# Performance work log

Measured on AMD Instinct MI355X. Metric: run time of the kernel, lower is better.

Reference implementation:

```python
import jax, jax.numpy as jnp
import numpy as np

SEQ, BATCH = 1024, 2
N_HEAD, D_MODEL = 16, 1024
Q_LORA, KV_LORA = 20, 20
ROPE = D_MODEL // N_HEAD // 2   # 32 qk_rope_head_dim
NOPE = D_MODEL // N_HEAD // 2   # 32 qk_nope_head_dim
V_DIM = D_MODEL // N_HEAD       # 64
N_EXP, HID = 4, 1024            # hidden_dim = d_inner//5 = 5120//5
N_GROUP, TOPK_GROUP, TOP_K = 2, 2, 1
ROUTED_SCALE = 1.0


def setup_inputs() -> dict:
    key = jax.random.key(0)
    ks = jax.random.split(key, 16)
    sc = 0.02
    return {
        'dec_inp': jax.random.normal(ks[0], (SEQ, BATCH, D_MODEL), jnp.float32),
        'wq_a': jax.random.normal(ks[1], (D_MODEL, Q_LORA), jnp.float32) * sc,
        'q_norm_w': jnp.ones((Q_LORA,), jnp.float32),
        'wq_b': jax.random.normal(ks[2], (Q_LORA, N_HEAD * (NOPE + ROPE)), jnp.float32) * sc,
        'wkv_a': jax.random.normal(ks[3], (D_MODEL, KV_LORA + ROPE), jnp.float32) * sc,
        'kv_norm_w': jnp.ones((KV_LORA,), jnp.float32),
        'wkv_b': jax.random.normal(ks[4], (KV_LORA, N_HEAD * (NOPE + V_DIM)), jnp.float32) * sc,
        'wo': jax.random.normal(ks[5], (N_HEAD * V_DIM, D_MODEL), jnp.float32) * sc,
        'gate_w': jax.random.normal(ks[6], (N_EXP, D_MODEL), jnp.float32) * sc,
        'exp_gate': jax.random.normal(ks[7], (N_EXP, D_MODEL, HID), jnp.float32) * sc,
        'exp_up': jax.random.normal(ks[8], (N_EXP, D_MODEL, HID), jnp.float32) * sc,
        'exp_down': jax.random.normal(ks[9], (N_EXP, HID, D_MODEL), jnp.float32) * sc,
        'sh_gate': jax.random.normal(ks[10], (D_MODEL, HID), jnp.float32) * sc,
        'sh_up': jax.random.normal(ks[11], (D_MODEL, HID), jnp.float32) * sc,
        'sh_down': jax.random.normal(ks[12], (HID, D_MODEL), jnp.float32) * sc,
    }


def _rms(x, w, eps=1e-6):
    return x * jax.lax.rsqrt(jnp.mean(x * x, axis=-1, keepdims=True) + eps) * w


def _freqs(seqlen):
    # precompute_freqs_cis(rope_dim * n_head, seqlen): dim = 512 here
    dim = ROPE * N_HEAD
    inv = 1.0 / (10000.0 ** (jnp.arange(0, dim, 2, dtype=jnp.float32) / dim))  # [dim//2]
    ang = jnp.arange(seqlen, dtype=jnp.float32)[:, None] * inv[None, :]       # [s, dim//2]
    ang = ang.reshape(seqlen, N_HEAD, ROPE // 2)
    return jnp.cos(ang), jnp.sin(ang)


def _rope(x, cos, sin):
    # x: [b, s, h, ROPE]; interleaved-pair complex rotation
    b, s, h, _ = x.shape
    xr = x.reshape(b, s, h, ROPE // 2, 2)
    x0, x1 = xr[..., 0], xr[..., 1]
    c = cos[None]  # [1, s, h, ROPE//2]
    sn = sin[None]
    o0 = x0 * c - x1 * sn
    o1 = x0 * sn + x1 * c
    return jnp.stack([o0, o1], axis=-1).reshape(b, s, h, ROPE)


def reference(dec_inp, wq_a, q_norm_w, wq_b, wkv_a, kv_norm_w, wkv_b, wo,
              gate_w, exp_gate, exp_up, exp_down, sh_gate, sh_up, sh_down):
    x = jnp.swapaxes(dec_inp, 0, 1)  # [b, s, d]
    b, s, d = x.shape
    # ---- MLA attention ----
    q = _rms(x @ wq_a, q_norm_w) @ wq_b                       # [b, s, h*(nope+rope)]
    q = q.reshape(b, s, N_HEAD, NOPE + ROPE)
    q_nope, q_pe = q[..., :NOPE], q[..., NOPE:]
    kv = x @ wkv_a                                            # [b, s, kv_lora+rope]
    ckv, k_pe = kv[..., :KV_LORA], kv[..., KV_LORA:]
    kvb = (_rms(ckv, kv_norm_w) @ wkv_b).reshape(b, s, N_HEAD, NOPE + V_DIM)
    k_nope, v = kvb[..., :NOPE], kvb[..., NOPE:]
    cos, sin = _freqs(s)
    q_pe = _rope(q_pe, cos, sin)
    k_pe_h = _rope(jnp.broadcast_to(k_pe[:, :, None, :], (b, s, N_HEAD, ROPE)), cos, sin)
    qf = jnp.concatenate([q_nope, q_pe], axis=-1)             # [b, s, h, 64]
    kf = jnp.concatenate([k_nope, k_pe_h], axis=-1)
    scale = 1.0 / np.sqrt(NOPE + ROPE)
    scores = jnp.einsum('bshd,bthd->bhst', qf, kf) * scale    # mask=None in the source forward
    probs = jax.nn.softmax(scores, axis=-1)
    attn = jnp.einsum('bhst,bthd->bshd', probs, v).reshape(b, s, N_HEAD * V_DIM)
    y = attn @ wo                                             # [b, s, d]
    y = jnp.swapaxes(y, 0, 1)                                 # [s, b, d]
    # ---- DeepSeekMoE (group_limited_greedy, top_k=1, 1 shared expert) ----
    xf = y.reshape(-1, d)                                     # [T, d]
    T = xf.shape[0]
    sc = jax.nn.softmax(xf @ gate_w.T, axis=-1)               # [T, E]
    gsc = sc.reshape(T, N_GROUP, N_EXP // N_GROUP).max(axis=-1)  # [T, n_group]
    _, gidx = jax.lax.top_k(gsc, TOPK_GROUP)
    gmask = jax.nn.one_hot(gidx, N_GROUP, dtype=sc.dtype).sum(axis=1)  # [T, n_group]
    smask = jnp.repeat(gmask, N_EXP // N_GROUP, axis=-1)      # [T, E]
    tw, ti = jax.lax.top_k(jnp.where(smask > 0, sc, 0.0), TOP_K)
    comb = (jax.nn.one_hot(ti, N_EXP, dtype=sc.dtype) * tw[..., None]).sum(axis=1) * ROUTED_SCALE  # [T, E]
    g = jnp.einsum('td,edh->teh', xf, exp_gate)
    u = jnp.einsum('td,edh->teh', xf, exp_up)
    dn = jnp.einsum('teh,ehd->ted', jax.nn.silu(g) * u, exp_down)
    routed = jnp.einsum('ted,te->td', dn, comb)
    shared = (jax.nn.silu(xf @ sh_gate) * (xf @ sh_up)) @ sh_down
    return (routed + shared).reshape(s, b, d)
```

## Files before the change

### kernel.cpp

```cpp
#include <hip/hip_runtime.h>
#include <hip/hip_bf16.h>
#include <math.h>

#define SEQ 1024
#define BATCH 2
#define T 2048
#define DM 1024
#define NH 16
#define NOPE 32
#define HD 64
#define QL 20
#define KVL 20
#define KVA 52
#define HID 1024
#define NEXP 4
#define LSTR 80

typedef short bf16x8 __attribute__((ext_vector_type(8)));
typedef float f32x4 __attribute__((ext_vector_type(4)));
typedef float f32x16 __attribute__((ext_vector_type(16)));
typedef __hip_bfloat16 bf16;

static __device__ __forceinline__ float sigmoidf_(float x) {
    return 1.0f / (1.0f + __expf(-x));
}
static __device__ __forceinline__ unsigned short bfbits(float x) {
    bf16 h = __float2bfloat16(x);
    return *reinterpret_cast<unsigned short*>(&h);
}
static __device__ __forceinline__ unsigned cvt_pk_bf16(float lo, float hi) {
    unsigned r;
    asm("v_cvt_pk_bf16_f32 %0, %1, %2" : "=v"(r) : "v"(lo), "v"(hi));
    return r;
}
static __device__ __forceinline__ void gload16(const bf16* g, char* l) {
    __builtin_amdgcn_global_load_lds(
        (const __attribute__((address_space(1))) unsigned int*)g,
        (__attribute__((address_space(3))) unsigned int*)l, 16, 0, 0);
}
static __device__ __forceinline__ void barrier_() {
    asm volatile("" ::: "memory");
    __builtin_amdgcn_s_barrier();
    asm volatile("" ::: "memory");
}
#define VMWAIT(N) asm volatile("s_waitcnt vmcnt(" #N ")" ::: "memory")

__global__ __launch_bounds__(256) void k_setup(
    const float* __restrict__ wo, const float* __restrict__ sg,
    const float* __restrict__ su, const float* __restrict__ sd,
    const float* __restrict__ eg, const float* __restrict__ eu,
    const float* __restrict__ ed,
    bf16* __restrict__ woT, bf16* __restrict__ sgT, bf16* __restrict__ suT,
    bf16* __restrict__ sdT, bf16* __restrict__ egT, bf16* __restrict__ euT,
    bf16* __restrict__ edT,
    const float* __restrict__ wq_a, const float* __restrict__ wkv_a,
    const float* __restrict__ wq_b, const float* __restrict__ wkv_b,
    bf16* __restrict__ loraT, bf16* __restrict__ wqbT, bf16* __restrict__ wkvbT,
    float* __restrict__ ctab, float* __restrict__ stab)
{
    int z = blockIdx.z;
    int tid = threadIdx.x;
    if (z < 16) {
        __shared__ float tile[32][33];
        const float* in; bf16* out;
        if      (z == 0) { in = wo; out = woT; }
        else if (z == 1) { in = sg; out = sgT; }
        else if (z == 2) { in = su; out = suT; }
        else if (z == 3) { in = sd; out = sdT; }
        else if (z < 8)  { size_t o = (size_t)(z - 4)  * DM * HID; in = eg + o; out = egT + o; }
        else if (z < 12) { size_t o = (size_t)(z - 8)  * DM * HID; in = eu + o; out = euT + o; }
        else             { size_t o = (size_t)(z - 12) * HID * DM; in = ed + o; out = edT + o; }
        int c0 = blockIdx.x * 32, r0 = blockIdx.y * 32;
        int tx = tid & 31, ty = tid >> 5;
        #pragma unroll
        for (int ii = 0; ii < 4; ++ii)
            tile[ty + ii * 8][tx] = in[(size_t)(r0 + ty + ii * 8) * 1024 + c0 + tx];
        __syncthreads();
        int c = tid >> 3, rg = (tid & 7) * 4;
        ushort4 o4;
        o4.x = bfbits(tile[rg + 0][c]);
        o4.y = bfbits(tile[rg + 1][c]);
        o4.z = bfbits(tile[rg + 2][c]);
        o4.w = bfbits(tile[rg + 3][c]);
        *(ushort4*)&out[(size_t)(c0 + c) * 1024 + r0 + rg] = o4;
    } else if (z == 16) {
        int s = blockIdx.y * 32 + blockIdx.x;
        int p = tid;
        float freq = exp2f(-(float)p * (13.287712379549449f / 256.0f));
        float ang = (float)s * freq;
        float sn, cs;
        __sincosf(ang, &sn, &cs);
        ctab[s * 256 + p] = cs;
        stab[s * 256 + p] = sn;
    } else {
        int idx = (blockIdx.y * 32 + blockIdx.x) * 256 + tid;
        if (z == 17) {
            if (idx >= 80 * 1024) return;
            int n = idx >> 10, k = idx & 1023;
            float v = (n < 20) ? wq_a[k * QL + n] : (n < 72 ? wkv_a[k * KVA + (n - 20)] : 0.f);
            loraT[idx] = __float2bfloat16(v);
        } else if (z == 18) {
            if (idx >= 1024 * 32) return;
            int n = idx >> 5, k = idx & 31;
            wqbT[idx] = __float2bfloat16(k < 20 ? wq_b[k * DM + n] : 0.f);
        } else {
            if (idx >= 1536 * 32) return;
            int n = idx >> 5, k = idx & 31;
            wkvbT[idx] = __float2bfloat16(k < 20 ? wkv_b[k * (NH * 96) + n] : 0.f);
        }
    }
}

__global__ __launch_bounds__(256) void k_p1(
    const float* __restrict__ dec, const bf16* __restrict__ loraT,
    float* __restrict__ lora4)
{
    __shared__ __align__(16) char As[128 * LSTR];
    __shared__ __align__(16) char Bs[80 * LSTR];
    const int tid = threadIdx.x;
    const int kz = blockIdx.x;
    const int m0 = blockIdx.y * 128;
    const int lane = tid & 63, wave = tid >> 6;
    const int g = lane >> 4, c = lane & 15;
    f32x4 acc[2][5] = {};
    for (int ks = 0; ks < 16; ++ks) {
        int k0 = kz * 512 + ks * 32;
        __syncthreads();
        #pragma unroll
        for (int pass = 0; pass < 4; ++pass) {
            int row = (tid >> 3) + pass * 32;
            int t = m0 + row;
            int b = t >> 10, s = t & 1023;
            f32x4 v = *(const f32x4*)&dec[(size_t)(s * 2 + b) * DM + k0 + (tid & 7) * 4];
            ushort4 h4;
            h4.x = bfbits(v[0]); h4.y = bfbits(v[1]);
            h4.z = bfbits(v[2]); h4.w = bfbits(v[3]);
            *(ushort4*)&As[row * LSTR + (tid & 7) * 8] = h4;
        }
        if (tid < 160) {
            int row = tid >> 1, hf = tid & 1;
            const bf16* src = &loraT[row * 1024 + k0 + hf * 16];
            *(int4*)&Bs[row * LSTR + hf * 32]      = *(const int4*)&src[0];
            *(int4*)&Bs[row * LSTR + hf * 32 + 16] = *(const int4*)&src[8];
        }
        __syncthreads();
        bf16x8 af[2], bff[5];
        #pragma unroll
        for (int mi = 0; mi < 2; ++mi)
            af[mi] = *(const bf16x8*)&As[(wave * 32 + mi * 16 + c) * LSTR + 16 * g];
        #pragma unroll
        for (int nf = 0; nf < 5; ++nf)
            bff[nf] = *(const bf16x8*)&Bs[(nf * 16 + c) * LSTR + 16 * g];
        #pragma unroll
        for (int mi = 0; mi < 2; ++mi)
            #pragma unroll
            for (int nf = 0; nf < 5; ++nf)
                acc[mi][nf] = __builtin_amdgcn_mfma_f32_16x16x32_bf16(af[mi], bff[nf], acc[mi][nf], 0, 0, 0);
    }
    #pragma unroll
    for (int mi = 0; mi < 2; ++mi)
        #pragma unroll
        for (int nf = 0; nf < 5; ++nf)
            #pragma unroll
            for (int r = 0; r < 4; ++r) {
                int col = nf * 16 + c;
                if (col < 72) {
                    int row = m0 + wave * 32 + mi * 16 + 4 * g + r;
                    lora4[((size_t)kz * T + row) * 72 + col] = acc[mi][nf][r];
                }
            }
}

__global__ __launch_bounds__(256) void k_p2m(
    const float* __restrict__ lora4, const float* __restrict__ qnw,
    const float* __restrict__ kvnw, const float* __restrict__ ctab,
    const float* __restrict__ stab, bf16* __restrict__ nrmq,
    bf16* __restrict__ nrmkv, bf16* __restrict__ kb, int* __restrict__ cnt)
{
    int bid = blockIdx.x, tid = threadIdx.x;
    if (bid == 0 && tid < 16) cnt[tid] = 0;
    {
        int t = bid, p = tid;
        int r = p & 15, h = p >> 4, s = t & (SEQ - 1);
        float y0 = lora4[t * 72 + 40 + 2 * r] + lora4[(size_t)(T + t) * 72 + 40 + 2 * r];
        float y1 = lora4[t * 72 + 41 + 2 * r] + lora4[(size_t)(T + t) * 72 + 41 + 2 * r];
        float cs = ctab[s * 256 + p], sn = stab[s * 256 + p];
        ushort2 pk;
        pk.x = bfbits(y0 * cs - y1 * sn);
        pk.y = bfbits(y0 * sn + y1 * cs);
        *(ushort2*)&kb[(size_t)t * DM + h * HD + NOPE + 2 * r] = pk;
    }
    if (bid < 8) {
        int t = bid * 256 + tid;
        float lq[20], lk[20];
        float ssq = 0.f, ssk = 0.f;
        #pragma unroll
        for (int i = 0; i < 20; ++i) {
            lq[i] = lora4[t * 72 + i] + lora4[(size_t)(T + t) * 72 + i];
            ssq += lq[i] * lq[i];
        }
        #pragma unroll
        for (int i = 0; i < 20; ++i) {
            lk[i] = lora4[t * 72 + 20 + i] + lora4[(size_t)(T + t) * 72 + 20 + i];
            ssk += lk[i] * lk[i];
        }
        float fq = rsqrtf(ssq / 20.f + 1e-6f);
        float fk = rsqrtf(ssk / 20.f + 1e-6f);
        #pragma unroll
        for (int i = 0; i < 32; ++i) {
            nrmq[t * 32 + i]  = __float2bfloat16(i < 20 ? lq[i] * fq * qnw[i]  : 0.f);
            nrmkv[t * 32 + i] = __float2bfloat16(i < 20 ? lk[i] * fk * kvnw[i] : 0.f);
        }
    }
}

__global__ __launch_bounds__(256) void k_p3(
    const bf16* __restrict__ nrmq, const bf16* __restrict__ wqbT,
    const bf16* __restrict__ nrmkv, const bf16* __restrict__ wkvbT,
    const float* __restrict__ ctab, const float* __restrict__ stab,
    bf16* __restrict__ qb, bf16* __restrict__ kb, bf16* __restrict__ vt_g)
{
    const int zq = (blockIdx.z == 0);
    if (zq && blockIdx.x >= 16) return;
    __shared__ __align__(16) char As[128 * LSTR];
    __shared__ __align__(16) char Bs[64 * LSTR];
    const int tid = threadIdx.x;
    const int m0 = blockIdx.y * 128, n0 = blockIdx.x * 64;
    const int lane = tid & 63, wave = tid >> 6;
    const int g = lane >> 4, c = lane & 15;
    const int wm = wave >> 1, wn = wave & 1;
    const bf16* nrm = zq ? nrmq : nrmkv;
    const bf16* wT  = zq ? wqbT : wkvbT;
    {
        int row = tid >> 1, hf = tid & 1;
        const bf16* sa = &nrm[(size_t)(m0 + row) * 32 + hf * 16];
        *(int4*)&As[row * LSTR + hf * 32]      = *(const int4*)&sa[0];
        *(int4*)&As[row * LSTR + hf * 32 + 16] = *(const int4*)&sa[8];
        int brow = tid >> 2;
        *(int4*)&Bs[brow * LSTR + (tid & 3) * 16] = *(const int4*)&wT[(size_t)(n0 + brow) * 32 + (tid & 3) * 8];
    }
    __syncthreads();
    f32x4 acc[4][2] = {};
    bf16x8 af[4], bfr[2];
    #pragma unroll
    for (int mi = 0; mi < 4; ++mi)
        af[mi] = *(const bf16x8*)&As[(wm * 64 + mi * 16 + c) * LSTR + 16 * g];
    #pragma unroll
    for (int ni = 0; ni < 2; ++ni)
        bfr[ni] = *(const bf16x8*)&Bs[(wn * 32 + ni * 16 + c) * LSTR + 16 * g];
    #pragma unroll
    for (int mi = 0; mi < 4; ++mi)
        #pragma unroll
        for (int ni = 0; ni < 2; ++ni)
            acc[mi][ni] = __builtin_amdgcn_mfma_f32_16x16x32_bf16(af[mi], bfr[ni], acc[mi][ni], 0, 0, 0);

    if (zq) {
        #pragma unroll
        for (int mi = 0; mi < 4; ++mi)
            #pragma unroll
            for (int ni = 0; ni < 2; ++ni) {
                #pragma unroll
                for (int r = 0; r < 4; ++r) acc[mi][ni][r] *= 0.18033688f;
                int n = n0 + wn * 32 + ni * 16 + c;
                int w = n & 63;
                if (w < 32) {
                    #pragma unroll
                    for (int r = 0; r < 4; ++r) {
                        int row = m0 + wm * 64 + mi * 16 + 4 * g + r;
                        qb[(size_t)row * DM + n] = __float2bfloat16(acc[mi][ni][r]);
                    }
                } else {
                    int h = n >> 6;
                    int pidx = h * 16 + ((w - 32) >> 1);
                    int odd = w & 1;
                    #pragma unroll
                    for (int r = 0; r < 4; ++r) {
                        int row = m0 + wm * 64 + mi * 16 + 4 * g + r;
                        int s = row & (SEQ - 1);
                        float own = acc[mi][ni][r];
                        float oth = __shfl_xor(own, 1);
                        float cs = ctab[s * 256 + pidx], sn = stab[s * 256 + pidx];
                        float o = odd ? (oth * sn + own * cs) : (own * cs - oth * sn);
                        qb[(size_t)row * DM + n] = __float2bfloat16(o);
                    }
                }
            }
    } else {
        #pragma unroll
        for (int mi = 0; mi < 4; ++mi)
            #pragma unroll
            for (int ni = 0; ni < 2; ++ni) {
                int n = n0 + wn * 32 + ni * 16 + c;
                int h = n / 96, w = n - h * 96;
                int row0 = m0 + wm * 64 + mi * 16 + 4 * g;
                if (w < NOPE) {
                    #pragma unroll
                    for (int r = 0; r < 4; ++r)
                        kb[(size_t)(row0 + r) * DM + h * HD + w] = __float2bfloat16(acc[mi][ni][r]);
                } else {
                    int d = w - NOPE;
                    int b = row0 >> 10, s0 = row0 & (SEQ - 1);
                    ushort4 v4;
                    v4.x = bfbits(acc[mi][ni][0]);
                    v4.y = bfbits(acc[mi][ni][1]);
                    v4.z = bfbits(acc[mi][ni][2]);
                    v4.w = bfbits(acc[mi][ni][3]);
                    *(ushort4*)&vt_g[(((size_t)(b * NH + h) * HD + d) << 10) + s0] = v4;
                }
            }
    }
}

__global__ __launch_bounds__(512) void k_attn(
    const bf16* __restrict__ qb, const bf16* __restrict__ kb,
    const bf16* __restrict__ vt_g, bf16* __restrict__ ab)
{
    __shared__ __align__(16) char stage[2][16384];
    __shared__ float pol[4][32][65];
    __shared__ float mll[4][32][2];

    const int qt = blockIdx.x, h = blockIdx.y, b = blockIdx.z;
    const int tid = threadIdx.x;
    const int lane = tid & 63, wave = tid >> 6;
    const int l31 = lane & 31, hi = lane >> 5;
    const int sp = wave >> 2, wq = wave & 3;
    const int q0 = qt * 128 + wq * 32;
    char* ks = stage[sp];
    char* vt = stage[sp] + 8192;
    const int ptid = tid & 255;

    bf16x8 qf[4];
    {
        const bf16* qrow = &qb[(size_t)(b * SEQ + q0 + l31) * DM + h * HD + 8 * hi];
        #pragma unroll
        for (int st = 0; st < 4; ++st)
            qf[st] = *(const bf16x8*)&qrow[16 * st];
    }

    f32x16 o0 = {}, o1 = {};
    float m_run = -3.0e38f, l_run = 0.f;
    const size_t vbase = ((size_t)(b * NH + h) * HD) << 10;

    for (int ktl = 0; ktl < 8; ++ktl) {
        const int kt = sp * 8 + ktl;
        __syncthreads();
        #pragma unroll
        for (int ps = 0; ps < 2; ++ps) {
            int row = (ptid >> 3) + ps * 32;
            int col8 = (ptid & 7) * 8;
            int sw = (col8 * 2) ^ ((row & 7) << 4);
            int4 kv4 = *(const int4*)&kb[(size_t)(b * SEQ + kt * 64 + row) * DM + h * HD + col8];
            *(int4*)&ks[row * 128 + sw] = kv4;
            int4 vv4 = *(const int4*)&vt_g[vbase + ((size_t)row << 10) + kt * 64 + col8];
            *(int4*)&vt[row * 128 + sw] = vv4;
        }
        __syncthreads();

        f32x16 sc0 = {}, sc1 = {};
        #pragma unroll
        for (int st = 0; st < 4; ++st) {
            int colb = 32 * st + 16 * hi;
            int r0 = l31;
            bf16x8 kf0 = *(const bf16x8*)&ks[r0 * 128 + (colb ^ ((r0 & 7) << 4))];
            sc0 = __builtin_amdgcn_mfma_f32_32x32x16_bf16(kf0, qf[st], sc0, 0, 0, 0);
            int r1 = 32 + l31;
            bf16x8 kf1 = *(const bf16x8*)&ks[r1 * 128 + (colb ^ ((r1 & 7) << 4))];
            sc1 = __builtin_amdgcn_mfma_f32_32x32x16_bf16(kf1, qf[st], sc1, 0, 0, 0);
        }

        float mt = fmaxf(sc0[0], sc1[0]);
        #pragma unroll
        for (int i = 1; i < 16; ++i) mt = fmaxf(mt, fmaxf(sc0[i], sc1[i]));
        mt = fmaxf(mt, __shfl_xor(mt, 32));

        if (!__all(mt <= m_run + 8.0f)) {
            float m_new = fmaxf(m_run, mt);
            float corr = exp2f(m_run - m_new);
            m_run = m_new;
            l_run *= corr;
            #pragma unroll
            for (int i = 0; i < 16; ++i) { o0[i] *= corr; o1[i] *= corr; }
        }
        float ls = 0.f;
        #pragma unroll
        for (int i = 0; i < 16; ++i) {
            sc0[i] = exp2f(sc0[i] - m_run);
            sc1[i] = exp2f(sc1[i] - m_run);
            ls += sc0[i] + sc1[i];
        }
        ls += __shfl_xor(ls, 32);
        l_run += ls;

        unsigned pk0[8], pk1[8];
        #pragma unroll
        for (int i = 0; i < 8; ++i) {
            pk0[i] = cvt_pk_bf16(sc0[2 * i], sc0[2 * i + 1]);
            pk1[i] = cvt_pk_bf16(sc1[2 * i], sc1[2 * i + 1]);
        }

#define PV_SUB(PK, KK)                                                          \
        {                                                                       \
            _Pragma("unroll")                                                   \
            for (int s = 0; s < 2; ++s) {                                       \
                unsigned sx = hi ? PK[4*s]   : PK[4*s+2];                       \
                unsigned rx = __shfl_xor(sx, 32);                               \
                unsigned sy = hi ? PK[4*s+1] : PK[4*s+3];                       \
                unsigned ry = __shfl_xor(sy, 32);                               \
                int4 bi;                                                        \
                bi.x = hi ? (int)rx : (int)PK[4*s];                             \
                bi.y = hi ? (int)ry : (int)PK[4*s+1];                           \
                bi.z = hi ? (int)PK[4*s+2] : (int)rx;                           \
                bi.w = hi ? (int)PK[4*s+3] : (int)ry;                           \
                bf16x8 bfr = *(bf16x8*)&bi;                                     \
                int cb = (KK) * 64 + 32 * s + 16 * hi;                          \
                {                                                               \
                    int vr = l31;                                               \
                    bf16x8 vf = *(const bf16x8*)&vt[vr * 128 + (cb ^ ((vr & 7) << 4))]; \
                    o0 = __builtin_amdgcn_mfma_f32_32x32x16_bf16(vf, bfr, o0, 0, 0, 0); \
                }                                                               \
                {                                                               \
                    int vr = 32 + l31;                                          \
                    bf16x8 vf = *(const bf16x8*)&vt[vr * 128 + (cb ^ ((vr & 7) << 4))]; \
                    o1 = __builtin_amdgcn_mfma_f32_32x32x16_bf16(vf, bfr, o1, 0, 0, 0); \
                }                                                               \
            }                                                                   \
        }
        PV_SUB(pk0, 0)
        PV_SUB(pk1, 1)
#undef PV_SUB
    }

    if (sp == 1) {
        #pragma unroll
        for (int i = 0; i < 16; ++i) {
            int d = (i & 3) + 8 * (i >> 2) + 4 * hi;
            pol[wq][l31][d]      = o0[i];
            pol[wq][l31][32 + d] = o1[i];
        }
        if (hi == 0) { mll[wq][l31][0] = m_run; mll[wq][l31][1] = l_run; }
    }
    __syncthreads();
    if (sp == 1) return;

    float m_b = mll[wq][l31][0], l_b = mll[wq][l31][1];
    float M = fmaxf(m_run, m_b);
    float wa = exp2f(m_run - M), wb = exp2f(m_b - M);
    float inv = 1.0f / (l_run * wa + l_b * wb);
    #pragma unroll
    for (int i = 0; i < 16; ++i) {
        int d = (i & 3) + 8 * (i >> 2) + 4 * hi;
        o0[i] = (o0[i] * wa + pol[wq][l31][d]      * wb) * inv;
        o1[i] = (o1[i] * wa + pol[wq][l31][32 + d] * wb) * inv;
    }

    char* tb = stage[0] + wq * 8192;
    #pragma unroll
    for (int i = 0; i < 8; ++i) {
        int dbase = 2 * (i & 1) + 8 * (i >> 1) + 4 * hi;
        *(unsigned*)&tb[l31 * 140 + (dbase) * 2]      = cvt_pk_bf16(o0[2 * i], o0[2 * i + 1]);
        *(unsigned*)&tb[l31 * 140 + (32 + dbase) * 2] = cvt_pk_bf16(o1[2 * i], o1[2 * i + 1]);
    }
    __builtin_amdgcn_s_waitcnt(0);
    #pragma unroll
    for (int p = 0; p < 8; ++p) {
        int idx = p * 64 + lane;
        int q = idx >> 4, c8 = idx & 15;
        int2 rv;
        rv.x = *(const int*)&tb[q * 140 + c8 * 8];
        rv.y = *(const int*)&tb[q * 140 + c8 * 8 + 4];
        *(int2*)&ab[(size_t)(b * SEQ + q0 + q) * DM + h * HD + c8 * 4] = rv;
    }
}

__global__ __launch_bounds__(512) void k_mm_plain(
    const bf16* __restrict__ A, const bf16* __restrict__ Bt, bf16* __restrict__ C)
{
    __shared__ __align__(16) char As[2][8192];
    __shared__ __align__(16) char Bs[2][4096];
    const int tid = threadIdx.x;
    const int lane = tid & 63, wave = tid >> 6;
    const int g = lane >> 4, c = lane & 15;
    const int wm = wave >> 1, wn = wave & 1;
    const int m0 = blockIdx.y * 128, n0 = blockIdx.x * 64;

    const int ldr = lane >> 2;
    const int ldc = (lane & 3) * 8;
    const bf16* agp = &A[(size_t)(m0 + wave * 16 + ldr) * DM + ldc];
    const bool doB = wave >= 4;
    const bf16* bgp = &Bt[(size_t)(n0 + (wave & 3) * 16 + ldr) * DM + ldc];
    const int aoffL = wave * 1024, boffL = (wave & 3) * 1024;

    f32x4 acc[2][2] = {};
    const int NT = DM / 32;
    gload16(agp, As[0] + aoffL);
    if (doB) gload16(bgp, Bs[0] + boffL);
    for (int k = 0; k < NT; ++k) {
        const int cur = k & 1;
        if (k + 1 < NT) {
            gload16(agp + (k + 1) * 32, As[cur ^ 1] + aoffL);
            if (doB) gload16(bgp + (k + 1) * 32, Bs[cur ^ 1] + boffL);
            if (doB) VMWAIT(2); else VMWAIT(1);
        } else {
            VMWAIT(0);
        }
        barrier_();
        bf16x8 af[2], bfx[2];
        #pragma unroll
        for (int mi = 0; mi < 2; ++mi)
            af[mi] = *(const bf16x8*)&As[cur][(wm * 32 + mi * 16 + c) * 64 + g * 16];
        #pragma unroll
        for (int ni = 0; ni < 2; ++ni)
            bfx[ni] = *(const bf16x8*)&Bs[cur][(wn * 32 + ni * 16 + c) * 64 + g * 16];
        #pragma unroll
        for (int mi = 0; mi < 2; ++mi)
            #pragma unroll
            for (int ni = 0; ni < 2; ++ni)
                acc[mi][ni] = __builtin_amdgcn_mfma_f32_16x16x32_bf16(af[mi], bfx[ni], acc[mi][ni], 0, 0, 0);
        barrier_();
    }
    #pragma unroll
    for (int mi = 0; mi < 2; ++mi)
        #pragma unroll
        for (int ni = 0; ni < 2; ++ni)
            #pragma unroll
            for (int r = 0; r < 4; ++r)
                C[(size_t)(m0 + wm * 32 + mi * 16 + 4 * g + r) * DM + n0 + wn * 32 + ni * 16 + c]
                    = __float2bfloat16(acc[mi][ni][r]);
}

__global__ __launch_bounds__(512) void k_mm_gu_all(
    const bf16* __restrict__ X, const bf16* __restrict__ egT,
    const bf16* __restrict__ euT, const bf16* __restrict__ sgT,
    const bf16* __restrict__ suT, const int* __restrict__ cnt,
    const int* __restrict__ lists, bf16* __restrict__ act_r,
    bf16* __restrict__ act_s)
{
    const int e = blockIdx.z;
    const bool SH = (e == 4);
    const int ntok = SH ? T : cnt[e];
    const int m0 = blockIdx.y * 128;
    if (m0 >= ntok) return;
    const int n0 = blockIdx.x * 64;
    __shared__ __align__(16) char As[2][8192];
    __shared__ __align__(16) char Bg[2][4096];
    __shared__ __align__(16) char Bu[2][4096];
    __shared__ int rowid[128];
    const int tid = threadIdx.x;
    if (tid < 128) {
        int idx = m0 + tid;
        rowid[tid] = SH ? idx : lists[e * T + (idx < ntok ? idx : ntok - 1)];
    }
    __syncthreads();
    const int lane = tid & 63, wave = tid >> 6;
    const int g = lane >> 4, c = lane & 15;
    const int wm = wave >> 1, wn = wave & 1;
    const bf16* Bge = SH ? sgT : egT + (size_t)e * HID * DM;
    const bf16* Bue = SH ? suT : euT + (size_t)e * HID * DM;
    bf16* act = SH ? act_s : act_r;

    const int ldr = lane >> 2;
    const int ldc = (lane & 3) * 8;
    const int myTok = rowid[wave * 16 + ldr];
    const bf16* agp = &X[(size_t)myTok * DM + ldc];
    const bool isG = wave < 4;
    const bf16* bgp = (isG ? Bge : Bue) + (size_t)(n0 + (wave & 3) * 16 + ldr) * DM + ldc;
    const int aoffL = wave * 1024, boffL = (wave & 3) * 1024;

    f32x4 accg[2][2] = {}, accu[2][2] = {};
    const int NT = DM / 32;
    gload16(agp, As[0] + aoffL);
    gload16(bgp, (isG ? Bg[0] : Bu[0]) + boffL);
    for (int k = 0; k < NT; ++k) {
        const int cur = k & 1;
        if (k + 1 < NT) {
            gload16(agp + (k + 1) * 32, As[cur ^ 1] + aoffL);
            gload16(bgp + (k + 1) * 32, (isG ? Bg[cur ^ 1] : Bu[cur ^ 1]) + boffL);
            VMWAIT(2);
        } else {
            VMWAIT(0);
        }
        barrier_();
        bf16x8 af[2], gf[2], uf[2];
        #pragma unroll
        for (int mi = 0; mi < 2; ++mi)
            af[mi] = *(const bf16x8*)&As[cur][(wm * 32 + mi * 16 + c) * 64 + g * 16];
        #pragma unroll
        for (int ni = 0; ni < 2; ++ni) {
            gf[ni] = *(const bf16x8*)&Bg[cur][(wn * 32 + ni * 16 + c) * 64 + g * 16];
            uf[ni] = *(const bf16x8*)&Bu[cur][(wn * 32 + ni * 16 + c) * 64 + g * 16];
        }
        #pragma unroll
        for (int mi = 0; mi < 2; ++mi)
            #pragma unroll
            for (int ni = 0; ni < 2; ++ni) {
                accg[mi][ni] = __builtin_amdgcn_mfma_f32_16x16x32_bf16(af[mi], gf[ni], accg[mi][ni], 0, 0, 0);
                accu[mi][ni] = __builtin_amdgcn_mfma_f32_16x16x32_bf16(af[mi], uf[ni], accu[mi][ni], 0, 0, 0);
            }
        barrier_();
    }
    #pragma unroll
    for (int mi = 0; mi < 2; ++mi)
        #pragma unroll
        for (int ni = 0; ni < 2; ++ni)
            #pragma unroll
            for (int r = 0; r < 4; ++r) {
                int lr = wm * 32 + mi * 16 + 4 * g + r;
                if (!SH && m0 + lr >= ntok) continue;
                int token = rowid[lr];
                float gv = accg[mi][ni][r], uv = accu[mi][ni][r];
                act[(size_t)token * HID + n0 + wn * 32 + ni * 16 + c] =
                    __float2bfloat16(gv * sigmoidf_(gv) * uv);
            }
}

__global__ __launch_bounds__(512) void k_mm_down_f(
    const bf16* __restrict__ Xr, const bf16* __restrict__ Xs,
    const bf16* __restrict__ edT, const bf16* __restrict__ sdT,
    const int* __restrict__ cnt, const int* __restrict__ lists,
    const float* __restrict__ wtok, float* __restrict__ out)
{
    const int e = blockIdx.z;
    const int ntok = cnt[e];
    const int m0 = blockIdx.y * 128;
    if (m0 >= ntok) return;
    const int n0 = blockIdx.x * 64;
    __shared__ __align__(16) char Ar[2][8192];
    __shared__ __align__(16) char Az[2][8192];
    __shared__ __align__(16) char Br[2][4096];
    __shared__ __align__(16) char Bz[2][4096];
    __shared__ int rowid[128];
    const int tid = threadIdx.x;
    if (tid < 128) {
        int idx = m0 + tid;
        rowid[tid] = lists[e * T + (idx < ntok ? idx : ntok - 1)];
    }
    __syncthreads();
    const int lane = tid & 63, wave = tid >> 6;
    const int g = lane >> 4, c = lane & 15;
    const int wm = wave >> 1, wn = wave & 1;
    const bf16* Bde = edT + (size_t)e * HID * DM;

    const int ldr = lane >> 2;
    const int ldc = (lane & 3) * 8;
    const int myTok = rowid[wave * 16 + ldr];
    const bf16* agr = &Xr[(size_t)myTok * HID + ldc];
    const bf16* ags = &Xs[(size_t)myTok * HID + ldc];
    const bool isR = wave < 4;
    const bf16* bgp = (isR ? Bde : sdT) + (size_t)(n0 + (wave & 3) * 16 + ldr) * HID + ldc;
    const int aoffL = wave * 1024, boffL = (wave & 3) * 1024;

    f32x4 accr[2][2] = {}, accs[2][2] = {};
    const int NT = HID / 32;
    gload16(agr, Ar[0] + aoffL);
    gload16(ags, Az[0] + aoffL);
    gload16(bgp, (isR ? Br[0] : Bz[0]) + boffL);
    for (int k = 0; k < NT; ++k) {
        const int cur = k & 1;
        if (k + 1 < NT) {
            gload16(agr + (k + 1) * 32, Ar[cur ^ 1] + aoffL);
            gload16(ags + (k + 1) * 32, Az[cur ^ 1] + aoffL);
            gload16(bgp + (k + 1) * 32, (isR ? Br[cur ^ 1] : Bz[cur ^ 1]) + boffL);
            VMWAIT(3);
        } else {
            VMWAIT(0);
        }
        barrier_();
        bf16x8 afr[2], afs[2], bfr[2], bfs[2];
        #pragma unroll
        for (int mi = 0; mi < 2; ++mi) {
            afr[mi] = *(const bf16x8*)&Ar[cur][(wm * 32 + mi * 16 + c) * 64 + g * 16];
            afs[mi] = *(const bf16x8*)&Az[cur][(wm * 32 + mi * 16 + c) * 64 + g * 16];
        }
        #pragma unroll
        for (int ni = 0; ni < 2; ++ni) {
            bfr[ni] = *(const bf16x8*)&Br[cur][(wn * 32 + ni * 16 + c) * 64 + g * 16];
            bfs[ni] = *(const bf16x8*)&Bz[cur][(wn * 32 + ni * 16 + c) * 64 + g * 16];
        }
        #pragma unroll
        for (int mi = 0; mi < 2; ++mi)
            #pragma unroll
            for (int ni = 0; ni < 2; ++ni) {
                accr[mi][ni] = __builtin_amdgcn_mfma_f32_16x16x32_bf16(afr[mi], bfr[ni], accr[mi][ni], 0, 0, 0);
                accs[mi][ni] = __builtin_amdgcn_mfma_f32_16x16x32_bf16(afs[mi], bfs[ni], accs[mi][ni], 0, 0, 0);
            }
        barrier_();
    }
    #pragma unroll
    for (int mi = 0; mi < 2; ++mi)
        #pragma unroll
        for (int ni = 0; ni < 2; ++ni)
            #pragma unroll
            for (int r = 0; r < 4; ++r) {
                int lr = wm * 32 + mi * 16 + 4 * g + r;
                if (m0 + lr >= ntok) continue;
                int token = rowid[lr];
                int bt = token >> 10, st = token & (SEQ - 1);
                size_t oo = (size_t)st * (BATCH * DM) + bt * DM + n0 + wn * 32 + ni * 16 + c;
                out[oo] = accr[mi][ni][r] * wtok[token] + accs[mi][ni][r];
            }
}

__global__ __launch_bounds__(256) void k_gate(
    const bf16* __restrict__ y, const float* __restrict__ gw,
    int* __restrict__ cnt, int* __restrict__ lists, float* __restrict__ wtok)
{
    int warp = threadIdx.x >> 6, lane = threadIdx.x & 63;
    int t = blockIdx.x * 4 + warp;
    float acc[NEXP] = {};
    for (int d = lane; d < DM; d += 64) {
        float xv = __bfloat162float(y[(size_t)t * DM + d]);
        #pragma unroll
        for (int e = 0; e < NEXP; ++e) acc[e] += xv * gw[e * DM + d];
    }
    #pragma unroll
    for (int off = 32; off; off >>= 1)
        #pragma unroll
        for (int e = 0; e < NEXP; ++e) acc[e] += __shfl_xor(acc[e], off);
    if (lane == 0) {
        float mx = fmaxf(fmaxf(acc[0], acc[1]), fmaxf(acc[2], acc[3]));
        float ex[NEXP], ssum = 0.f;
        #pragma unroll
        for (int e = 0; e < NEXP; ++e) { ex[e] = __expf(acc[e] - mx); ssum += ex[e]; }
        int best = 0; float bv = ex[0];
        #pragma unroll
        for (int e = 1; e < NEXP; ++e) if (ex[e] > bv) { bv = ex[e]; best = e; }
        wtok[t] = bv / ssum;
        int pos = atomicAdd(&cnt[best], 1);
        lists[best * T + pos] = t;
    }
}

extern "C" void kernel_launch(void* const* d_in, const int* in_sizes, int n_in,
                              void* d_out, int out_size, void* d_ws, size_t ws_size,
                              hipStream_t stream) {
    (void)in_sizes; (void)n_in; (void)out_size; (void)ws_size;
    const float* dec      = (const float*)d_in[0];
    const float* wq_a     = (const float*)d_in[1];
    const float* q_norm_w = (const float*)d_in[2];
    const float* wq_b     = (const float*)d_in[3];
    const float* wkv_a    = (const float*)d_in[4];
    const float* kv_norm_w= (const float*)d_in[5];
    const float* wkv_b    = (const float*)d_in[6];
    const float* wo       = (const float*)d_in[7];
    const float* gate_w   = (const float*)d_in[8];
    const float* exp_gate = (const float*)d_in[9];
    const float* exp_up   = (const float*)d_in[10];
    const float* exp_down = (const float*)d_in[11];
    const float* sh_gate  = (const float*)d_in[12];
    const float* sh_up    = (const float*)d_in[13];
    const float* sh_down  = (const float*)d_in[14];
    float* out = (float*)d_out;

    char* W = (char*)d_ws;
    bf16* qb   = (bf16*)(W);
    bf16* kb   = (bf16*)(W + (4ull  << 20));
    bf16* vt_g = (bf16*)(W + (8ull  << 20));
    char* SMALL = W + (12ull << 20);
    bf16* ab   = (bf16*)(W + (12ull << 20));
    bf16* woT = (bf16*)(W + (16ull << 20));
    bf16* sgT = (bf16*)(W + (18ull << 20));
    bf16* suT = (bf16*)(W + (20ull << 20));
    bf16* sdT = (bf16*)(W + (22ull << 20));
    bf16* egT = (bf16*)(W + (24ull << 20));
    bf16* euT = (bf16*)(W + (32ull << 20));
    bf16* edT = (bf16*)(W + (40ull << 20));
    int*   cnt   = (int*)(W + (48ull << 20));
    int*   lists = cnt + 16;
    float* wtok  = (float*)(lists + NEXP * T);
    bf16* yb    = qb;
    bf16* act_r = kb;
    bf16* act_s = vt_g;

    float* lora4 = (float*)(SMALL);
    bf16*  loraT = (bf16*) (SMALL + 1179648);
    bf16*  wqbT  = (bf16*) (SMALL + 1343488);
    bf16*  wkvbT = (bf16*) (SMALL + 1409024);
    bf16*  nrmq  = (bf16*) (SMALL + 1507328);
    bf16*  nrmkv = (bf16*) (SMALL + 1638400);
    float* ctab  = (float*)(SMALL + 1769472);
    float* stab  = (float*)(SMALL + 2818048);

    k_setup<<<dim3(32, 32, 20), 256, 0, stream>>>(
        wo, sh_gate, sh_up, sh_down, exp_gate, exp_up, exp_down,
        woT, sgT, suT, sdT, egT, euT, edT,
        wq_a, wkv_a, wq_b, wkv_b, loraT, wqbT, wkvbT, ctab, stab);

    k_p1<<<dim3(2, 16), 256, 0, stream>>>(dec, loraT, lora4);
    k_p2m<<<T, 256, 0, stream>>>(lora4, q_norm_w, kv_norm_w, ctab, stab,
                                 nrmq, nrmkv, kb, cnt);
    k_p3<<<dim3(24, 16, 2), 256, 0, stream>>>(nrmq, wqbT, nrmkv, wkvbT,
                                              ctab, stab, qb, kb, vt_g);

    k_attn<<<dim3(SEQ / 128, NH, BATCH), 512, 0, stream>>>(qb, kb, vt_g, ab);
    k_mm_plain<<<dim3(DM / 64, T / 128), 512, 0, stream>>>(ab, woT, yb);
    k_gate<<<T / 4, 256, 0, stream>>>(yb, gate_w, cnt, lists, wtok);
    k_mm_gu_all<<<dim3(HID / 64, T / 128, NEXP + 1), 512, 0, stream>>>(
        yb, egT, euT, sgT, suT, cnt, lists, act_r, act_s);
    k_mm_down_f<<<dim3(DM / 64, T / 128, NEXP), 512, 0, stream>>>(
        act_r, act_s, edT, sdT, cnt, lists, wtok, out);
}
```

Measured before the change: 183.9 us.

## Prefetch attention K/V tiles, widen GEMM K-step, swizzle block order

The attention kernel now loads the next K/V tile into registers while the current one is being consumed, so global load latency overlaps with compute. The plain and gate/up GEMMs now stage 64-wide K tiles (double the LDS) with an XOR swizzle, which halves the number of barrier iterations. All four kernels remap block indices so blocks that run together share tiles and get better L2 locality. The costs are higher register and LDS use, which may lower occupancy.

```diff
diff --git a/kernel.cpp b/kernel.cpp
--- a/kernel.cpp
+++ b/kernel.cpp
@@ -319,7 +319,10 @@
     __shared__ float pol[4][32][65];
     __shared__ float mll[4][32][2];
 
-    const int qt = blockIdx.x, h = blockIdx.y, b = blockIdx.z;
+    const int orig = blockIdx.y * 8 + blockIdx.x;
+    const int h  = (orig & 7) * 2 + ((orig >> 3) & 1);
+    const int qt = orig >> 4;
+    const int b = blockIdx.z;
     const int tid = threadIdx.x;
     const int lane = tid & 63, wave = tid >> 6;
     const int l31 = lane & 31, hi = lane >> 5;
@@ -328,6 +331,7 @@
     char* ks = stage[sp];
     char* vt = stage[sp] + 8192;
     const int ptid = tid & 255;
+    const int prow0 = ptid >> 3, pcol8 = (ptid & 7) * 8;
 
     bf16x8 qf[4];
     {
@@ -341,19 +345,28 @@
     float m_run = -3.0e38f, l_run = 0.f;
     const size_t vbase = ((size_t)(b * NH + h) * HD) << 10;
 
+    int4 pk_[2], pv_[2];
+#define LOADT(KT)                                                               \
+    {                                                                           \
+        _Pragma("unroll")                                                       \
+        for (int ps = 0; ps < 2; ++ps) {                                        \
+            int row = prow0 + ps * 32;                                          \
+            pk_[ps] = *(const int4*)&kb[(size_t)(b * SEQ + (KT) * 64 + row) * DM + h * HD + pcol8]; \
+            pv_[ps] = *(const int4*)&vt_g[vbase + ((size_t)row << 10) + (KT) * 64 + pcol8]; \
+        }                                                                       \
+    }
+    LOADT(sp * 8)
+
     for (int ktl = 0; ktl < 8; ++ktl) {
-        const int kt = sp * 8 + ktl;
         __syncthreads();
         #pragma unroll
         for (int ps = 0; ps < 2; ++ps) {
-            int row = (ptid >> 3) + ps * 32;
-            int col8 = (ptid & 7) * 8;
-            int sw = (col8 * 2) ^ ((row & 7) << 4);
-            int4 kv4 = *(const int4*)&kb[(size_t)(b * SEQ + kt * 64 + row) * DM + h * HD + col8];
-            *(int4*)&ks[row * 128 + sw] = kv4;
-            int4 vv4 = *(const int4*)&vt_g[vbase + ((size_t)row << 10) + kt * 64 + col8];
-            *(int4*)&vt[row * 128 + sw] = vv4;
-        }
+            int row = prow0 + ps * 32;
+            int sw = (pcol8 * 2) ^ ((row & 7) << 4);
+            *(int4*)&ks[row * 128 + sw] = pk_[ps];
+            *(int4*)&vt[row * 128 + sw] = pv_[ps];
+        }
+        if (ktl < 7) LOADT(sp * 8 + ktl + 1)
         __syncthreads();
 
         f32x16 sc0 = {}, sc1 = {};
@@ -429,6 +442,7 @@
         PV_SUB(pk1, 1)
 #undef PV_SUB
     }
+#undef LOADT
 
     if (sp == 1) {
         #pragma unroll
@@ -475,47 +489,57 @@
 __global__ __launch_bounds__(512) void k_mm_plain(
     const bf16* __restrict__ A, const bf16* __restrict__ Bt, bf16* __restrict__ C)
 {
-    __shared__ __align__(16) char As[2][8192];
-    __shared__ __align__(16) char Bs[2][4096];
+    __shared__ __align__(16) char As[2][16384];
+    __shared__ __align__(16) char Bs[2][8192];
     const int tid = threadIdx.x;
     const int lane = tid & 63, wave = tid >> 6;
     const int g = lane >> 4, c = lane & 15;
     const int wm = wave >> 1, wn = wave & 1;
-    const int m0 = blockIdx.y * 128, n0 = blockIdx.x * 64;
-
-    const int ldr = lane >> 2;
-    const int ldc = (lane & 3) * 8;
-    const bf16* agp = &A[(size_t)(m0 + wave * 16 + ldr) * DM + ldc];
-    const bool doB = wave >= 4;
-    const bf16* bgp = &Bt[(size_t)(n0 + (wave & 3) * 16 + ldr) * DM + ldc];
-    const int aoffL = wave * 1024, boffL = (wave & 3) * 1024;
+    int orig = blockIdx.y * 16 + blockIdx.x;
+    int swz = (orig & 7) * 32 + (orig >> 3);
+    const int n0 = (swz & 15) * 64, m0 = (swz >> 4) * 128;
+
+    const int lr = lane >> 3, c16 = lane & 7;
+    const int sc16 = c16 ^ ((lr & 1) << 2);
+    const bf16* agp0 = &A[(size_t)(m0 + wave * 16 + lr) * DM + sc16 * 8];
+    const bf16* agp1 = &A[(size_t)(m0 + wave * 16 + 8 + lr) * DM + sc16 * 8];
+    const bf16* bgp  = &Bt[(size_t)(n0 + wave * 8 + lr) * DM + sc16 * 8];
 
     f32x4 acc[2][2] = {};
-    const int NT = DM / 32;
-    gload16(agp, As[0] + aoffL);
-    if (doB) gload16(bgp, Bs[0] + boffL);
+    const int NT = DM / 64;
+    gload16(agp0, As[0] + wave * 2048);
+    gload16(agp1, As[0] + wave * 2048 + 1024);
+    gload16(bgp,  Bs[0] + wave * 1024);
     for (int k = 0; k < NT; ++k) {
         const int cur = k & 1;
         if (k + 1 < NT) {
-            gload16(agp + (k + 1) * 32, As[cur ^ 1] + aoffL);
-            if (doB) gload16(bgp + (k + 1) * 32, Bs[cur ^ 1] + boffL);
-            if (doB) VMWAIT(2); else VMWAIT(1);
+            gload16(agp0 + (k + 1) * 64, As[cur ^ 1] + wave * 2048);
+            gload16(agp1 + (k + 1) * 64, As[cur ^ 1] + wave * 2048 + 1024);
+            gload16(bgp  + (k + 1) * 64, Bs[cur ^ 1] + wave * 1024);
+            VMWAIT(3);
         } else {
             VMWAIT(0);
         }
         barrier_();
-        bf16x8 af[2], bfx[2];
-        #pragma unroll
-        for (int mi = 0; mi < 2; ++mi)
-            af[mi] = *(const bf16x8*)&As[cur][(wm * 32 + mi * 16 + c) * 64 + g * 16];
-        #pragma unroll
-        for (int ni = 0; ni < 2; ++ni)
-            bfx[ni] = *(const bf16x8*)&Bs[cur][(wn * 32 + ni * 16 + c) * 64 + g * 16];
-        #pragma unroll
-        for (int mi = 0; mi < 2; ++mi)
-            #pragma unroll
-            for (int ni = 0; ni < 2; ++ni)
-                acc[mi][ni] = __builtin_amdgcn_mfma_f32_16x16x32_bf16(af[mi], bfx[ni], acc[mi][ni], 0, 0, 0);
+        #pragma unroll
+        for (int ks = 0; ks < 2; ++ks) {
+            bf16x8 af[2], bfx[2];
+            #pragma unroll
+            for (int mi = 0; mi < 2; ++mi) {
+                int R = wm * 32 + mi * 16 + c;
+                af[mi] = *(const bf16x8*)&As[cur][R * 128 + ((ks ^ (R & 1)) << 6) + g * 16];
+            }
+            #pragma unroll
+            for (int ni = 0; ni < 2; ++ni) {
+                int R = wn * 32 + ni * 16 + c;
+                bfx[ni] = *(const bf16x8*)&Bs[cur][R * 128 + ((ks ^ (R & 1)) << 6) + g * 16];
+            }
+            #pragma unroll
+            for (int mi = 0; mi < 2; ++mi)
+                #pragma unroll
+                for (int ni = 0; ni < 2; ++ni)
+                    acc[mi][ni] = __builtin_amdgcn_mfma_f32_16x16x32_bf16(af[mi], bfx[ni], acc[mi][ni], 0, 0, 0);
+        }
         barrier_();
     }
     #pragma unroll
@@ -538,12 +562,13 @@
     const int e = blockIdx.z;
     const bool SH = (e == 4);
     const int ntok = SH ? T : cnt[e];
-    const int m0 = blockIdx.y * 128;
+    int orig = blockIdx.y * 16 + blockIdx.x;
+    int swz = (orig & 7) * 32 + (orig >> 3);
+    const int n0 = (swz & 15) * 64, m0 = (swz >> 4) * 128;
     if (m0 >= ntok) return;
-    const int n0 = blockIdx.x * 64;
-    __shared__ __align__(16) char As[2][8192];
-    __shared__ __align__(16) char Bg[2][4096];
-    __shared__ __align__(16) char Bu[2][4096];
+    __shared__ __align__(16) char As[2][16384];
+    __shared__ __align__(16) char Bg[2][8192];
+    __shared__ __align__(16) char Bu[2][8192];
     __shared__ int rowid[128];
     const int tid = threadIdx.x;
     if (tid < 128) {
@@ -558,44 +583,63 @@
     const bf16* Bue = SH ? suT : euT + (size_t)e * HID * DM;
     bf16* act = SH ? act_s : act_r;
 
-    const int ldr = lane >> 2;
-    const int ldc = (lane & 3) * 8;
-    const int myTok = rowid[wave * 16 + ldr];
-    const bf16* agp = &X[(size_t)myTok * DM + ldc];
+    const int lr = lane >> 3, c16 = lane & 7;
+    const int sc16 = c16 ^ ((lr & 1) << 2);
+    const int tokA0 = rowid[wave * 16 + lr];
+    const int tokA1 = rowid[wave * 16 + 8 + lr];
+    const bf16* agp0 = &X[(size_t)tokA0 * DM + sc16 * 8];
+    const bf16* agp1 = &X[(size_t)tokA1 * DM + sc16 * 8];
     const bool isG = wave < 4;
-    const bf16* bgp = (isG ? Bge : Bue) + (size_t)(n0 + (wave & 3) * 16 + ldr) * DM + ldc;
-    const int aoffL = wave * 1024, boffL = (wave & 3) * 1024;
+    const bf16* bbase = isG ? Bge : Bue;
+    const int w4 = wave & 3;
+    const bf16* bgp0 = &bbase[(size_t)(n0 + w4 * 16 + lr) * DM + sc16 * 8];
+    const bf16* bgp1 = &bbase[(size_t)(n0 + w4 * 16 + 8 + lr) * DM + sc16 * 8];
 
     f32x4 accg[2][2] = {}, accu[2][2] = {};
-    const int NT = DM / 32;
-    gload16(agp, As[0] + aoffL);
-    gload16(bgp, (isG ? Bg[0] : Bu[0]) + boffL);
+    const int NT = DM / 64;
+    {
+        char* bl = (isG ? Bg[0] : Bu[0]) + w4 * 2048;
+        gload16(agp0, As[0] + wave * 2048);
+        gload16(agp1, As[0] + wave * 2048 + 1024);
+        gload16(bgp0, bl);
+        gload16(bgp1, bl + 1024);
+    }
     for (int k = 0; k < NT; ++k) {
         const int cur = k & 1;
         if (k + 1 < NT) {
-            gload16(agp + (k + 1) * 32, As[cur ^ 1] + aoffL);
-            gload16(bgp + (k + 1) * 32, (isG ? Bg[cur ^ 1] : Bu[cur ^ 1]) + boffL);
-            VMWAIT(2);
+            char* bl = (isG ? Bg[cur ^ 1] : Bu[cur ^ 1]) + w4 * 2048;
+            gload16(agp0 + (k + 1) * 64, As[cur ^ 1] + wave * 2048);
+            gload16(agp1 + (k + 1) * 64, As[cur ^ 1] + wave * 2048 + 1024);
+            gload16(bgp0 + (k + 1) * 64, bl);
+            gload16(bgp1 + (k + 1) * 64, bl + 1024);
+            VMWAIT(4);
         } else {
             VMWAIT(0);
         }
         barrier_();
-        bf16x8 af[2], gf[2], uf[2];
-        #pragma unroll
-        for (int mi = 0; mi < 2; ++mi)
-            af[mi] = *(const bf16x8*)&As[cur][(wm * 32 + mi * 16 + c) * 64 + g * 16];
-        #pragma unroll
-        for (int ni = 0; ni < 2; ++ni) {
-            gf[ni] = *(const bf16x8*)&Bg[cur][(wn * 32 + ni * 16 + c) * 64 + g * 16];
-            uf[ni] = *(const bf16x8*)&Bu[cur][(wn * 32 + ni * 16 + c) * 64 + g * 16];
-        }
-        #pragma unroll
-        for (int mi = 0; mi < 2; ++mi)
+        #pragma unroll
+        for (int ks = 0; ks < 2; ++ks) {
+            bf16x8 af[2], gf[2], uf[2];
+            #pragma unroll
+            for (int mi = 0; mi < 2; ++mi) {
+                int R = wm * 32 + mi * 16 + c;
+                af[mi] = *(const bf16x8*)&As[cur][R * 128 + ((ks ^ (R & 1)) << 6) + g * 16];
+            }
             #pragma unroll
             for (int ni = 0; ni < 2; ++ni) {
-                accg[mi][ni] = __builtin_amdgcn_mfma_f32_16x16x32_bf16(af[mi], gf[ni], accg[mi][ni], 0, 0, 0);
-                accu[mi][ni] = __builtin_amdgcn_mfma_f32_16x16x32_bf16(af[mi], uf[ni], accu[mi][ni], 0, 0, 0);
-            }
+                int R = wn * 32 + ni * 16 + c;
+                int off = R * 128 + ((ks ^ (R & 1)) << 6) + g * 16;
+                gf[ni] = *(const bf16x8*)&Bg[cur][off];
+                uf[ni] = *(const bf16x8*)&Bu[cur][off];
+            }
+            #pragma unroll
+            for (int mi = 0; mi < 2; ++mi)
+                #pragma unroll
+                for (int ni = 0; ni < 2; ++ni) {
+                    accg[mi][ni] = __builtin_amdgcn_mfma_f32_16x16x32_bf16(af[mi], gf[ni], accg[mi][ni], 0, 0, 0);
+                    accu[mi][ni] = __builtin_amdgcn_mfma_f32_16x16x32_bf16(af[mi], uf[ni], accu[mi][ni], 0, 0, 0);
+                }
+        }
         barrier_();
     }
     #pragma unroll
@@ -604,9 +648,9 @@
         for (int ni = 0; ni < 2; ++ni)
             #pragma unroll
             for (int r = 0; r < 4; ++r) {
-                int lr = wm * 32 + mi * 16 + 4 * g + r;
-                if (!SH && m0 + lr >= ntok) continue;
-                int token = rowid[lr];
+                int lrr = wm * 32 + mi * 16 + 4 * g + r;
+                if (!SH && m0 + lrr >= ntok) continue;
+                int token = rowid[lrr];
                 float gv = accg[mi][ni][r], uv = accu[mi][ni][r];
                 act[(size_t)token * HID + n0 + wn * 32 + ni * 16 + c] =
                     __float2bfloat16(gv * sigmoidf_(gv) * uv);
@@ -621,9 +665,10 @@
 {
     const int e = blockIdx.z;
     const int ntok = cnt[e];
-    const int m0 = blockIdx.y * 128;
+    int orig = blockIdx.y * 16 + blockIdx.x;
+    int swz = (orig & 7) * 32 + (orig >> 3);
+    const int n0 = (swz & 15) * 64, m0 = (swz >> 4) * 128;
     if (m0 >= ntok) return;
-    const int n0 = blockIdx.x * 64;
     __shared__ __align__(16) char Ar[2][8192];
     __shared__ __align__(16) char Az[2][8192];
     __shared__ __align__(16) char Br[2][4096];
@@ -791,11 +836,11 @@
     k_p3<<<dim3(24, 16, 2), 256, 0, stream>>>(nrmq, wqbT, nrmkv, wkvbT,
                                               ctab, stab, qb, kb, vt_g);
 
-    k_attn<<<dim3(SEQ / 128, NH, BATCH), 512, 0, stream>>>(qb, kb, vt_g, ab);
-    k_mm_plain<<<dim3(DM / 64, T / 128), 512, 0, stream>>>(ab, woT, yb);
+    k_attn<<<dim3(8, 16, BATCH), 512, 0, stream>>>(qb, kb, vt_g, ab);
+    k_mm_plain<<<dim3(16, 16), 512, 0, stream>>>(ab, woT, yb);
     k_gate<<<T / 4, 256, 0, stream>>>(yb, gate_w, cnt, lists, wtok);
-    k_mm_gu_all<<<dim3(HID / 64, T / 128, NEXP + 1), 512, 0, stream>>>(
+    k_mm_gu_all<<<dim3(16, 16, NEXP + 1), 512, 0, stream>>>(
         yb, egT, euT, sgT, suT, cnt, lists, act_r, act_s);
-    k_mm_down_f<<<dim3(DM / 64, T / 128, NEXP), 512, 0, stream>>>(
+    k_mm_down_f<<<dim3(16, 16, NEXP), 512, 0, stream>>>(
         act_r, act_s, edT, sdT, cnt, lists, wtok, out);
 }
```

After: 198.3 us. 7.9% more time.
